# Performance work log

Hardware: AMD Instinct MI355X
Metric: run time of the kernel (lower is better)

Reference implementation:

```python
import jax, jax.numpy as jnp
import numpy as np

R = 65  # num_relations


def rgcn_conv(x, edge_index, edge_type, W, root, bias):
    """PyG RGCNConv with per-relation mean aggregation.
    Aggregate-then-transform (linearity lets us swap the order):
      mean_r[n] = mean over edges e with type r, dst(e)=n of x[src(e)]
      out = sum_r mean_r @ W_r + x @ root + bias
    """
    N = x.shape[0]
    src, dst = edge_index[0], edge_index[1]
    seg = edge_type * N + dst  # composite (relation, dst) segment id
    sums = jax.ops.segment_sum(x[src], seg, num_segments=R * N)
    sums = sums.reshape(R, N, -1)  # [R, N, F]
    cnt = jax.ops.segment_sum(jnp.ones(src.shape, x.dtype), seg, num_segments=R * N)
    cnt = cnt.reshape(R, N, 1)
    mean = sums / jnp.maximum(cnt, 1.0)
    return jnp.einsum('rni,rio->no', mean, W) + x @ root + bias


def setup_inputs() -> dict:
    key = jax.random.key(0)
    ks = jax.random.split(key, 20)
    N, E, F_in, H, M = 8000, 192000, 64, 256, 64
    B = 128
    inp = {
        'x': jax.random.normal(ks[0], (N, F_in), jnp.float32),
        'edge_index': jax.random.randint(ks[1], (2, E), 0, N),
        'edge_type': jax.random.randint(ks[2], (E,), 0, R),
        'batch': jnp.sort(jax.random.randint(ks[3], (N,), 0, B)),
    }
    def glorot(k, shape):
        fan = shape[-2] + shape[-1]
        return jax.random.normal(k, shape, jnp.float32) * jnp.sqrt(2.0 / fan)
    inp['W1'] = glorot(ks[4], (R, F_in, H)); inp['root1'] = glorot(ks[5], (F_in, H)); inp['b1'] = jnp.zeros((H,), jnp.float32)
    inp['W2'] = glorot(ks[6], (R, H, H));   inp['root2'] = glorot(ks[7], (H, H));   inp['b2'] = jnp.zeros((H,), jnp.float32)
    inp['W3'] = glorot(ks[8], (R, H, H));   inp['root3'] = glorot(ks[9], (H, H));   inp['b3'] = jnp.zeros((H,), jnp.float32)
    inp['ws_w'] = glorot(ks[10], (H, 1));    inp['ws_b'] = jnp.zeros((1,), jnp.float32)
    inp['m_w1'] = glorot(ks[11], (H, M)); inp['m_b1'] = jnp.zeros((M,), jnp.float32)
    inp['m_w2'] = glorot(ks[12], (M, M)); inp['m_b2'] = jnp.zeros((M,), jnp.float32)
    inp['m_w3'] = glorot(ks[13], (M, 1)); inp['m_b3'] = jnp.zeros((1,), jnp.float32)
    return inp


def reference(x, edge_index, edge_type, batch,
              W1, root1, b1, W2, root2, b2, W3, root3, b3,
              ws_w, ws_b, m_w1, m_b1, m_w2, m_b2, m_w3, m_b3):
    B = 128  # number of graphs in the batch
    h = jax.nn.relu(rgcn_conv(x, edge_index, edge_type, W1, root1, b1))
    h = jax.nn.relu(rgcn_conv(h, edge_index, edge_type, W2, root2, b2))
    h = jax.nn.relu(rgcn_conv(h, edge_index, edge_type, W3, root3, b3))
    # WeightedSum pooling: sigmoid gate per node, scatter-sum per graph
    w = jax.nn.sigmoid(h @ ws_w + ws_b)            # [N, 1]
    pooled = jax.ops.segment_sum(w * h, batch, num_segments=B)  # [B, H]
    # MLP head
    m = jax.nn.relu(pooled @ m_w1 + m_b1)
    m = jax.nn.relu(m @ m_w2 + m_b2)
    return m @ m_w3 + m_b3                          # [B, 1]
```

## Files before the change

### kernel.cpp

```cpp
#include <hip/hip_runtime.h>

#define NNODES 8000
#define NEDGES 192000
#define NREL   65
#define RP     66
#define HDIM   256
#define FDIM   64
#define NGRAPH 128
#define MDIM   64
#define TILE_M 64
#define MAXT   3456
#define EPTOT  (NEDGES + NNODES)

typedef _Float16 half8 __attribute__((ext_vector_type(8)));
typedef _Float16 half4 __attribute__((ext_vector_type(4)));
typedef float    f32x4 __attribute__((ext_vector_type(4)));


__global__ void count_kernel(const int* __restrict__ ei, const int* __restrict__ et,
                             int* __restrict__ cnt_rn, int* __restrict__ type_cnt,
                             int* __restrict__ ddeg) {
    __shared__ int lbin[NREL];
    int tid = threadIdx.x;
    if (tid < NREL) lbin[tid] = 0;
    __syncthreads();
    int e = blockIdx.x * 256 + tid;
    if (e < NEDGES) {
        int t = et[e];
        int d = ei[NEDGES + e];
        atomicAdd(&lbin[t], 1);
        atomicAdd(&cnt_rn[t * NNODES + d], 1);
        atomicAdd(&ddeg[d], 1);
    }
    __syncthreads();
    if (tid < NREL && lbin[tid] > 0) atomicAdd(&type_cnt[tid], lbin[tid]);
}

__global__ void scan_tiles_kernel(const int* __restrict__ type_cnt, int* __restrict__ type_off,
                                  int* __restrict__ tile_rel, int* __restrict__ tile_start,
                                  int* __restrict__ tile_nrows) {
    __shared__ int s_off[RP + 1];
    __shared__ int s_toff[RP + 1];
    if (threadIdx.x == 0) {
        int off = 0, toff = 0;
        for (int r = 0; r < RP; r++) {
            int c = (r < NREL) ? type_cnt[r] : NNODES;
            s_off[r] = off; s_toff[r] = toff;
            off += c; toff += (c + TILE_M - 1) / TILE_M;
        }
        s_off[RP] = off; s_toff[RP] = toff;
        type_off[RP] = off;
    }
    __syncthreads();
    int r = threadIdx.x;
    if (r < RP) {
        type_off[r] = s_off[r];
        int c = s_off[r + 1] - s_off[r];
        int nt = (c + TILE_M - 1) / TILE_M;
        for (int i = 0; i < nt; i++) {
            int idx = s_toff[r] + i;
            tile_rel[idx]   = r;
            tile_start[idx] = s_off[r] + i * TILE_M;
            tile_nrows[idx] = min(TILE_M, c - i * TILE_M);
        }
    }
}

__global__ void dst_scan_kernel(const int* __restrict__ ddeg, int* __restrict__ dst_off) {
    __shared__ int part[256];
    int t = threadIdx.x;
    int base = t * 32;
    int s = 0;
    for (int i = 0; i < 32; i++) {
        int n = base + i;
        if (n < NNODES) s += ddeg[n] + 1;
    }
    part[t] = s;
    __syncthreads();
    if (t == 0) {
        int run = 0;
        for (int i = 0; i < 256; i++) { int tmp = part[i]; part[i] = run; run += tmp; }
        dst_off[NNODES] = run;
    }
    __syncthreads();
    int run = part[t];
    for (int i = 0; i < 32; i++) {
        int n = base + i;
        if (n < NNODES) { dst_off[n] = run; run += ddeg[n] + 1; }
    }
}

__global__ void scatter_kernel(const int* __restrict__ ei, const int* __restrict__ et,
                               const int* __restrict__ cnt_rn, const int* __restrict__ type_off,
                               int* __restrict__ type_cur,
                               const int* __restrict__ dst_off, int* __restrict__ dst_cur,
                               int* __restrict__ esrc, int* __restrict__ eq,
                               float* __restrict__ escale) {
    __shared__ int lbin[NREL];
    __shared__ int gbase[NREL];
    int tid = threadIdx.x;
    if (tid < NREL) lbin[tid] = 0;
    __syncthreads();
    int i = blockIdx.x * 256 + tid;
    int t = 0, lrank = 0;
    bool is_edge = (i < NEDGES);
    if (is_edge) {
        t = et[i];
        lrank = atomicAdd(&lbin[t], 1);
    }
    __syncthreads();
    if (tid < NREL && lbin[tid] > 0) gbase[tid] = atomicAdd(&type_cur[tid], lbin[tid]);
    __syncthreads();
    if (is_edge) {
        int d = ei[NEDGES + i];
        int p = type_off[t] + gbase[t] + lrank;
        int q = dst_off[d] + atomicAdd(&dst_cur[d], 1);
        esrc[p] = ei[i];
        eq[p] = q;
        escale[p] = 1.0f / (float)cnt_rn[t * NNODES + d];
    } else if (i < EPTOT) {
        int n = i - NEDGES;
        int p = NEDGES + n;
        int q = dst_off[n] + atomicAdd(&dst_cur[n], 1);
        esrc[p] = n; eq[p] = q; escale[p] = 1.0f;
    }
}

__global__ void convW_kernel(const float* __restrict__ W, const float* __restrict__ root,
                             _Float16* __restrict__ Wt, int K) {
    int r = blockIdx.x, k0 = blockIdx.y * 32, n0 = blockIdx.z * 32;
    const float* src = (r < NREL) ? (W + (size_t)r * K * HDIM) : root;
    __shared__ float tile[32][33];
    int tj = threadIdx.x & 31, ti = threadIdx.x >> 5;
    #pragma unroll
    for (int s = 0; s < 4; s++) {
        int i = ti + s * 8;
        tile[i][tj] = src[(size_t)(k0 + i) * HDIM + n0 + tj];
    }
    __syncthreads();
    #pragma unroll
    for (int s = 0; s < 4; s++) {
        int i = ti + s * 8;
        Wt[((size_t)r * HDIM + (n0 + i)) * K + k0 + tj] = (_Float16)tile[tj][i];
    }
}

__global__ void conv_x_kernel(const float* __restrict__ x, _Float16* __restrict__ x16) {
    int i = blockIdx.x * 256 + threadIdx.x;
    if (i < NNODES * FDIM) x16[i] = (_Float16)x[i];
}

template <int K>
__global__ __launch_bounds__(256)
void edge_gemm_kernel(const _Float16* __restrict__ hin, const _Float16* __restrict__ Wt,
                      const int* __restrict__ esrc, const int* __restrict__ eq,
                      const float* __restrict__ escale,
                      const int* __restrict__ tile_rel, const int* __restrict__ tile_start,
                      const int* __restrict__ tile_nrows,
                      _Float16* __restrict__ Y) {
    int nr = tile_nrows[blockIdx.x];
    if (nr == 0) return;
    int r  = tile_rel[blockIdx.x];
    int ts = tile_start[blockIdx.x];

    constexpr int LK = K + 8;
    constexpr int SO = HDIM + 8;
    constexpr int LMAX = (LK > SO) ? LK : SO;
    __shared__ _Float16 sbuf[TILE_M * LMAX];
    __shared__ int   sq[TILE_M];
    __shared__ float sscale[TILE_M];

    int tid = threadIdx.x;
    constexpr int CPR = K / 8;
    for (int idx = tid; idx < TILE_M * CPR; idx += 256) {
        int row = idx / CPR, c = idx % CPR;
        uint4 v = make_uint4(0, 0, 0, 0);
        if (row < nr) {
            int src = esrc[ts + row];
            v = *(const uint4*)(hin + (size_t)src * K + c * 8);
        }
        *(uint4*)&sbuf[row * LK + c * 8] = v;
    }
    if (tid < TILE_M) {
        if (tid < nr) { sq[tid] = eq[ts + tid]; sscale[tid] = escale[ts + tid]; }
        else          { sq[tid] = 0;            sscale[tid] = 0.f; }
    }
    __syncthreads();

    int lane = tid & 63, w = tid >> 6;
    int lm = lane & 15, quad = lane >> 4;
    f32x4 acc[4][4] = {};
    const _Float16* Bbase = Wt + ((size_t)r * HDIM + w * 64 + lm) * K + quad * 8;
    const _Float16* Abase = sbuf + lm * LK + quad * 8;

    for (int kk = 0; kk < K; kk += 32) {
        half8 a[4], b[4];
        #pragma unroll
        for (int mt = 0; mt < 4; mt++)
            a[mt] = *(const half8*)(Abase + mt * 16 * LK + kk);
        #pragma unroll
        for (int nt = 0; nt < 4; nt++)
            b[nt] = *(const half8*)(Bbase + nt * 16 * K + kk);
        #pragma unroll
        for (int mt = 0; mt < 4; mt++)
            #pragma unroll
            for (int nt = 0; nt < 4; nt++)
                acc[mt][nt] = __builtin_amdgcn_mfma_f32_16x16x32_f16(a[mt], b[nt], acc[mt][nt], 0, 0, 0);
    }

    __syncthreads();

    #pragma unroll
    for (int mt = 0; mt < 4; mt++) {
        #pragma unroll
        for (int rr = 0; rr < 4; rr++) {
            int row = mt * 16 + quad * 4 + rr;
            float s = sscale[row];
            #pragma unroll
            for (int nt = 0; nt < 4; nt++) {
                int col = w * 64 + nt * 16 + lm;
                sbuf[row * SO + col] = (_Float16)(acc[mt][nt][rr] * s);
            }
        }
    }
    __syncthreads();

    for (int idx = tid; idx < TILE_M * 32; idx += 256) {
        int row = idx >> 5, seg = idx & 31;
        if (row < nr) {
            uint4 v = *(const uint4*)&sbuf[row * SO + seg * 8];
            *(uint4*)(Y + (size_t)sq[row] * HDIM + seg * 8) = v;
        }
    }
}

__global__ __launch_bounds__(256)
void reduce_kernel(const _Float16* __restrict__ Y, const int* __restrict__ dst_off,
                   const float* __restrict__ bias, _Float16* __restrict__ hout) {
    int n = blockIdx.x;
    int start = dst_off[n], end = dst_off[n + 1];
    int t = threadIdx.x;
    int c = t & 31;
    int r = t >> 5;
    float acc[8] = {0, 0, 0, 0, 0, 0, 0, 0};
    for (int j = start + r; j < end; j += 8) {
        half8 v = *(const half8*)(Y + (size_t)j * HDIM + c * 8);
        #pragma unroll
        for (int k = 0; k < 8; k++) acc[k] += (float)v[k];
    }
    __shared__ float red[8][32][8];
    #pragma unroll
    for (int k = 0; k < 8; k++) red[r][c][k] = acc[k];
    __syncthreads();
    if (t < 32) {
        float a[8];
        #pragma unroll
        for (int k = 0; k < 8; k++) a[k] = red[0][t][k];
        for (int rr = 1; rr < 8; rr++)
            #pragma unroll
            for (int k = 0; k < 8; k++) a[k] += red[rr][t][k];
        half8 o;
        #pragma unroll
        for (int k = 0; k < 8; k++) {
            float v = a[k] + bias[t * 8 + k];
            o[k] = (_Float16)(v > 0.f ? v : 0.f);
        }
        *(half8*)(hout + (size_t)n * HDIM + t * 8) = o;
    }
}


__global__ void gate_kernel(const _Float16* __restrict__ h, const float* __restrict__ ws_w,
                            const float* __restrict__ ws_b, float* __restrict__ gate) {
    int node = blockIdx.x * 4 + (threadIdx.x >> 6);
    int lane = threadIdx.x & 63;
    half4 v = *(const half4*)(h + (size_t)node * HDIM + lane * 4);
    float s = 0.f;
    #pragma unroll
    for (int k = 0; k < 4; k++) s += (float)v[k] * ws_w[lane * 4 + k];
    for (int o = 32; o > 0; o >>= 1) s += __shfl_down(s, o, 64);
    if (lane == 0) gate[node] = 1.f / (1.f + __expf(-(s + ws_b[0])));
}

__global__ void pool_kernel(const _Float16* __restrict__ h, const float* __restrict__ gate,
                            const int* __restrict__ batch, float* __restrict__ pooled) {
    int g = blockIdx.x, t = threadIdx.x;
    int a = 0, b = NNODES;
    while (a < b) { int m = (a + b) >> 1; if (batch[m] < g) a = m + 1; else b = m; }
    int lo = a;
    b = NNODES;
    while (a < b) { int m = (a + b) >> 1; if (batch[m] < g + 1) a = m + 1; else b = m; }
    int hi = a;
    float acc = 0.f;
    for (int n = lo; n < hi; n++)
        acc += gate[n] * (float)h[(size_t)n * HDIM + t];
    pooled[(size_t)g * HDIM + t] = acc;
}

__global__ void head_kernel(const float* __restrict__ pooled,
                            const float* __restrict__ w1, const float* __restrict__ b1,
                            const float* __restrict__ w2, const float* __restrict__ b2,
                            const float* __restrict__ w3, const float* __restrict__ b3,
                            float* __restrict__ out) {
    int b = blockIdx.x, tid = threadIdx.x;
    __shared__ float sp[HDIM];
    __shared__ float m1[MDIM];
    __shared__ float m2[MDIM];
    for (int i = tid; i < HDIM; i += 64) sp[i] = pooled[(size_t)b * HDIM + i];
    __syncthreads();
    float a = b1[tid];
    for (int i = 0; i < HDIM; i++) a += sp[i] * w1[i * MDIM + tid];
    m1[tid] = a > 0.f ? a : 0.f;
    __syncthreads();
    float c = b2[tid];
    for (int i = 0; i < MDIM; i++) c += m1[i] * w2[i * MDIM + tid];
    m2[tid] = c > 0.f ? c : 0.f;
    __syncthreads();
    float p = m2[tid] * w3[tid];
    for (int o = 32; o > 0; o >>= 1) p += __shfl_down(p, o, 64);
    if (tid == 0) out[b] = p + b3[0];
}


extern "C" void kernel_launch(void* const* d_in, const int* in_sizes, int n_in,
                              void* d_out, int out_size, void* d_ws, size_t ws_size,
                              hipStream_t stream) {
    const float* x     = (const float*)d_in[0];
    const int*   ei    = (const int*)d_in[1];
    const int*   et    = (const int*)d_in[2];
    const int*   batch = (const int*)d_in[3];
    const float* W1    = (const float*)d_in[4];
    const float* root1 = (const float*)d_in[5];
    const float* b1    = (const float*)d_in[6];
    const float* W2    = (const float*)d_in[7];
    const float* root2 = (const float*)d_in[8];
    const float* b2    = (const float*)d_in[9];
    const float* W3    = (const float*)d_in[10];
    const float* root3 = (const float*)d_in[11];
    const float* b3    = (const float*)d_in[12];
    const float* ws_w  = (const float*)d_in[13];
    const float* ws_b  = (const float*)d_in[14];
    const float* m_w1  = (const float*)d_in[15];
    const float* m_b1  = (const float*)d_in[16];
    const float* m_w2  = (const float*)d_in[17];
    const float* m_b2  = (const float*)d_in[18];
    const float* m_w3  = (const float*)d_in[19];
    const float* m_b3  = (const float*)d_in[20];
    float* out = (float*)d_out;

    char* ws = (char*)d_ws;
    size_t o = 0;
    auto take = [&](size_t bytes) { size_t r = o; o = (o + bytes + 255) & ~(size_t)255; return r; };

    size_t o_cnt_rn = take((size_t)NREL * NNODES * 4);
    size_t o_tcnt   = take(RP * 4);
    size_t o_tcur   = take(RP * 4);
    size_t o_toff   = take((RP + 1) * 4);
    size_t o_ddeg   = take((size_t)NNODES * 4);
    size_t o_dcur   = take((size_t)NNODES * 4);
    size_t o_doff   = take((size_t)(NNODES + 1) * 4);
    size_t o_esrc   = take((size_t)EPTOT * 4);
    size_t o_eq     = take((size_t)EPTOT * 4);
    size_t o_escale = take((size_t)EPTOT * 4);
    size_t o_trel   = take(MAXT * 4);
    size_t o_tstart = take(MAXT * 4);
    size_t o_tnrows = take(MAXT * 4);
    size_t o_wt1    = take((size_t)RP * HDIM * FDIM * 2);
    size_t o_wt2    = take((size_t)RP * HDIM * HDIM * 2);
    size_t o_wt3    = take((size_t)RP * HDIM * HDIM * 2);
    size_t o_x16    = take((size_t)NNODES * FDIM * 2);
    size_t o_h16    = take((size_t)NNODES * HDIM * 2);
    size_t o_gate   = take((size_t)NNODES * 4);
    size_t o_pool   = take((size_t)NGRAPH * HDIM * 4);
    size_t o_y16    = take((size_t)EPTOT * HDIM * 2);

    int*      cnt_rn   = (int*)(ws + o_cnt_rn);
    int*      type_cnt = (int*)(ws + o_tcnt);
    int*      type_cur = (int*)(ws + o_tcur);
    int*      type_off = (int*)(ws + o_toff);
    int*      ddeg     = (int*)(ws + o_ddeg);
    int*      dst_cur  = (int*)(ws + o_dcur);
    int*      dst_off  = (int*)(ws + o_doff);
    int*      esrc     = (int*)(ws + o_esrc);
    int*      eq       = (int*)(ws + o_eq);
    float*    escale   = (float*)(ws + o_escale);
    int*      trel     = (int*)(ws + o_trel);
    int*      tstart   = (int*)(ws + o_tstart);
    int*      tnrows   = (int*)(ws + o_tnrows);
    _Float16* Wt1      = (_Float16*)(ws + o_wt1);
    _Float16* Wt2      = (_Float16*)(ws + o_wt2);
    _Float16* Wt3      = (_Float16*)(ws + o_wt3);
    _Float16* x16      = (_Float16*)(ws + o_x16);
    _Float16* h16      = (_Float16*)(ws + o_h16);
    float*    gate     = (float*)(ws + o_gate);
    float*    pooled   = (float*)(ws + o_pool);
    _Float16* Y16      = (_Float16*)(ws + o_y16);

    hipMemsetAsync(ws + o_cnt_rn, 0, o_toff - o_cnt_rn, stream);
    hipMemsetAsync(ws + o_ddeg, 0, o_doff - o_ddeg, stream);
    hipMemsetAsync(ws + o_tnrows, 0, MAXT * 4, stream);

    count_kernel<<<(NEDGES + 255) / 256, 256, 0, stream>>>(ei, et, cnt_rn, type_cnt, ddeg);
    scan_tiles_kernel<<<1, 128, 0, stream>>>(type_cnt, type_off, trel, tstart, tnrows);
    dst_scan_kernel<<<1, 256, 0, stream>>>(ddeg, dst_off);
    scatter_kernel<<<(EPTOT + 255) / 256, 256, 0, stream>>>(ei, et, cnt_rn, type_off, type_cur,
                                                            dst_off, dst_cur, esrc, eq, escale);

    convW_kernel<<<dim3(RP, FDIM / 32, HDIM / 32), 256, 0, stream>>>(W1, root1, Wt1, FDIM);
    convW_kernel<<<dim3(RP, HDIM / 32, HDIM / 32), 256, 0, stream>>>(W2, root2, Wt2, HDIM);
    convW_kernel<<<dim3(RP, HDIM / 32, HDIM / 32), 256, 0, stream>>>(W3, root3, Wt3, HDIM);
    conv_x_kernel<<<(NNODES * FDIM + 255) / 256, 256, 0, stream>>>(x, x16);

    edge_gemm_kernel<FDIM><<<MAXT, 256, 0, stream>>>(x16, Wt1, esrc, eq, escale,
                                                     trel, tstart, tnrows, Y16);
    reduce_kernel<<<NNODES, 256, 0, stream>>>(Y16, dst_off, b1, h16);

    edge_gemm_kernel<HDIM><<<MAXT, 256, 0, stream>>>(h16, Wt2, esrc, eq, escale,
                                                     trel, tstart, tnrows, Y16);
    reduce_kernel<<<NNODES, 256, 0, stream>>>(Y16, dst_off, b2, h16);

    edge_gemm_kernel<HDIM><<<MAXT, 256, 0, stream>>>(h16, Wt3, esrc, eq, escale,
                                                     trel, tstart, tnrows, Y16);
    reduce_kernel<<<NNODES, 256, 0, stream>>>(Y16, dst_off, b3, h16);

    gate_kernel<<<NNODES / 4, 256, 0, stream>>>(h16, ws_w, ws_b, gate);
    pool_kernel<<<NGRAPH, 256, 0, stream>>>(h16, gate, batch, pooled);
    head_kernel<<<NGRAPH, 64, 0, stream>>>(pooled, m_w1, m_b1, m_w2, m_b2, m_w3, m_b3, out);

    (void)in_sizes; (void)n_in; (void)out_size; (void)ws_size;
}
```

Baseline: 490.9 us.

## Shrink edge GEMM LDS footprint, swizzle tile order, use nontemporal Y traffic

The edge GEMM kernel now stages the gathered A rows in K-chunks of at most 128 and writes the output tile back in two 32-row halves, which shrinks the shared-memory buffer and should allow more blocks per CU. The block-to-tile mapping is interleaved across eight strides, which spreads relations and tile sizes more evenly across the grid. Stores to Y and the loads in the reduce kernel now use nontemporal hints to avoid polluting cache with streamed intermediate data. The cost is extra barriers per chunk and half, and the interleaved mapping assumes the grid size equals MAXT.

Measured after the change: 503.9 us. 1.03x slower.

```diff
diff --git a/kernel.cpp b/kernel.cpp
--- a/kernel.cpp
+++ b/kernel.cpp
@@ -15,6 +15,7 @@
 typedef _Float16 half8 __attribute__((ext_vector_type(8)));
 typedef _Float16 half4 __attribute__((ext_vector_type(4)));
 typedef float    f32x4 __attribute__((ext_vector_type(4)));
+typedef unsigned int u32x4 __attribute__((ext_vector_type(4)));
 
 
 __global__ void count_kernel(const int* __restrict__ ei, const int* __restrict__ et,
@@ -158,34 +159,29 @@
                       const int* __restrict__ tile_rel, const int* __restrict__ tile_start,
                       const int* __restrict__ tile_nrows,
                       _Float16* __restrict__ Y) {
-    int nr = tile_nrows[blockIdx.x];
+    int bid  = blockIdx.x;
+    int tile = (bid & 7) * (MAXT / 8) + (bid >> 3);
+
+    int nr = tile_nrows[tile];
     if (nr == 0) return;
-    int r  = tile_rel[blockIdx.x];
-    int ts = tile_start[blockIdx.x];
-
-    constexpr int LK = K + 8;
-    constexpr int SO = HDIM + 8;
-    constexpr int LMAX = (LK > SO) ? LK : SO;
-    __shared__ _Float16 sbuf[TILE_M * LMAX];
+    int r  = tile_rel[tile];
+    int ts = tile_start[tile];
+
+    constexpr int KH  = (K > 128) ? 128 : K;
+    constexpr int LK  = KH + 8;
+    constexpr int SO  = HDIM + 8;
+    constexpr int AEL = TILE_M * LK;
+    constexpr int OEL = 32 * SO;
+    constexpr int EL  = (AEL > OEL) ? AEL : OEL;
+    __shared__ _Float16 sbuf[EL];
     __shared__ int   sq[TILE_M];
     __shared__ float sscale[TILE_M];
 
     int tid = threadIdx.x;
-    constexpr int CPR = K / 8;
-    for (int idx = tid; idx < TILE_M * CPR; idx += 256) {
-        int row = idx / CPR, c = idx % CPR;
-        uint4 v = make_uint4(0, 0, 0, 0);
-        if (row < nr) {
-            int src = esrc[ts + row];
-            v = *(const uint4*)(hin + (size_t)src * K + c * 8);
-        }
-        *(uint4*)&sbuf[row * LK + c * 8] = v;
-    }
     if (tid < TILE_M) {
         if (tid < nr) { sq[tid] = eq[ts + tid]; sscale[tid] = escale[ts + tid]; }
         else          { sq[tid] = 0;            sscale[tid] = 0.f; }
     }
-    __syncthreads();
 
     int lane = tid & 63, w = tid >> 6;
     int lm = lane & 15, quad = lane >> 4;
@@ -193,44 +189,63 @@
     const _Float16* Bbase = Wt + ((size_t)r * HDIM + w * 64 + lm) * K + quad * 8;
     const _Float16* Abase = sbuf + lm * LK + quad * 8;
 
-    for (int kk = 0; kk < K; kk += 32) {
-        half8 a[4], b[4];
-        #pragma unroll
-        for (int mt = 0; mt < 4; mt++)
-            a[mt] = *(const half8*)(Abase + mt * 16 * LK + kk);
-        #pragma unroll
-        for (int nt = 0; nt < 4; nt++)
-            b[nt] = *(const half8*)(Bbase + nt * 16 * K + kk);
-        #pragma unroll
-        for (int mt = 0; mt < 4; mt++)
+    constexpr int CPR = KH / 8;
+    for (int kh = 0; kh < K; kh += KH) {
+        for (int idx = tid; idx < TILE_M * CPR; idx += 256) {
+            int row = idx / CPR, c = idx % CPR;
+            u32x4 v = {0, 0, 0, 0};
+            if (row < nr) {
+                int src = esrc[ts + row];
+                v = *(const u32x4*)(hin + (size_t)src * K + kh + c * 8);
+            }
+            *(u32x4*)&sbuf[row * LK + c * 8] = v;
+        }
+        __syncthreads();
+
+        for (int kk = 0; kk < KH; kk += 32) {
+            half8 a[4], b[4];
+            #pragma unroll
+            for (int mt = 0; mt < 4; mt++)
+                a[mt] = *(const half8*)(Abase + mt * 16 * LK + kk);
             #pragma unroll
             for (int nt = 0; nt < 4; nt++)
-                acc[mt][nt] = __builtin_amdgcn_mfma_f32_16x16x32_f16(a[mt], b[nt], acc[mt][nt], 0, 0, 0);
-    }
-
-    __syncthreads();
+                b[nt] = *(const half8*)(Bbase + nt * 16 * K + kh + kk);
+            #pragma unroll
+            for (int mt = 0; mt < 4; mt++)
+                #pragma unroll
+                for (int nt = 0; nt < 4; nt++)
+                    acc[mt][nt] = __builtin_amdgcn_mfma_f32_16x16x32_f16(a[mt], b[nt], acc[mt][nt], 0, 0, 0);
+        }
+        __syncthreads();
+    }
 
     #pragma unroll
-    for (int mt = 0; mt < 4; mt++) {
+    for (int h = 0; h < 2; h++) {
         #pragma unroll
-        for (int rr = 0; rr < 4; rr++) {
-            int row = mt * 16 + quad * 4 + rr;
-            float s = sscale[row];
+        for (int mh = 0; mh < 2; mh++) {
+            int mt = h * 2 + mh;
             #pragma unroll
-            for (int nt = 0; nt < 4; nt++) {
-                int col = w * 64 + nt * 16 + lm;
-                sbuf[row * SO + col] = (_Float16)(acc[mt][nt][rr] * s);
+            for (int rr = 0; rr < 4; rr++) {
+                int row  = mt * 16 + quad * 4 + rr;
+                int lrow = row - h * 32;
+                float s = sscale[row];
+                #pragma unroll
+                for (int nt = 0; nt < 4; nt++) {
+                    int col = w * 64 + nt * 16 + lm;
+                    sbuf[lrow * SO + col] = (_Float16)(acc[mt][nt][rr] * s);
+                }
             }
         }
-    }
-    __syncthreads();
-
-    for (int idx = tid; idx < TILE_M * 32; idx += 256) {
-        int row = idx >> 5, seg = idx & 31;
-        if (row < nr) {
-            uint4 v = *(const uint4*)&sbuf[row * SO + seg * 8];
-            *(uint4*)(Y + (size_t)sq[row] * HDIM + seg * 8) = v;
-        }
+        __syncthreads();
+        for (int idx = tid; idx < 32 * 32; idx += 256) {
+            int lrow = idx >> 5, seg = idx & 31;
+            int row = h * 32 + lrow;
+            if (row < nr) {
+                u32x4 v = *(const u32x4*)&sbuf[lrow * SO + seg * 8];
+                __builtin_nontemporal_store(v, (u32x4*)(Y + (size_t)sq[row] * HDIM + seg * 8));
+            }
+        }
+        if (h == 0) __syncthreads();
     }
 }
 
@@ -244,7 +259,8 @@
     int r = t >> 5;
     float acc[8] = {0, 0, 0, 0, 0, 0, 0, 0};
     for (int j = start + r; j < end; j += 8) {
-        half8 v = *(const half8*)(Y + (size_t)j * HDIM + c * 8);
+        u32x4 u = __builtin_nontemporal_load((const u32x4*)(Y + (size_t)j * HDIM + c * 8));
+        half8 v = *(half8*)&u;
         #pragma unroll
         for (int k = 0; k < 8; k++) acc[k] += (float)v[k];
     }
```

## Load gathered A rows directly from global and use per-wave epilogue scratch

Applied to the files above, without the earlier changes.

The edge GEMM stops staging gathered source rows in shared memory and has each lane load its A fragments straight from global memory via per-row source indices. The epilogue writes into a per-wave scratch buffer, so no block-wide barriers are needed, and Y is written and read with nontemporal stores and loads. Tile order is also swizzled across block ids, and launch bounds request three blocks per CU. This removes the LDS staging pass and the syncs, but every wave now re-reads the gathered rows from global or cache.

After: 615.5 us. +25.4%, slower.

```diff
diff --git a/kernel.cpp b/kernel.cpp
--- a/kernel.cpp
+++ b/kernel.cpp
@@ -15,6 +15,7 @@
 typedef _Float16 half8 __attribute__((ext_vector_type(8)));
 typedef _Float16 half4 __attribute__((ext_vector_type(4)));
 typedef float    f32x4 __attribute__((ext_vector_type(4)));
+typedef unsigned int u32x4 __attribute__((ext_vector_type(4)));
 
 
 __global__ void count_kernel(const int* __restrict__ ei, const int* __restrict__ et,
@@ -151,56 +152,44 @@
 }
 
 template <int K>
-__global__ __launch_bounds__(256)
+__global__ __launch_bounds__(256, 3)
 void edge_gemm_kernel(const _Float16* __restrict__ hin, const _Float16* __restrict__ Wt,
                       const int* __restrict__ esrc, const int* __restrict__ eq,
                       const float* __restrict__ escale,
                       const int* __restrict__ tile_rel, const int* __restrict__ tile_start,
                       const int* __restrict__ tile_nrows,
                       _Float16* __restrict__ Y) {
-    int nr = tile_nrows[blockIdx.x];
+    int bid  = blockIdx.x;
+    int tile = (bid & 7) * (MAXT / 8) + (bid >> 3);
+
+    int nr = tile_nrows[tile];
     if (nr == 0) return;
-    int r  = tile_rel[blockIdx.x];
-    int ts = tile_start[blockIdx.x];
-
-    constexpr int LK = K + 8;
-    constexpr int SO = HDIM + 8;
-    constexpr int LMAX = (LK > SO) ? LK : SO;
-    __shared__ _Float16 sbuf[TILE_M * LMAX];
-    __shared__ int   sq[TILE_M];
-    __shared__ float sscale[TILE_M];
+    int r  = tile_rel[tile];
+    int ts = tile_start[tile];
 
     int tid = threadIdx.x;
-    constexpr int CPR = K / 8;
-    for (int idx = tid; idx < TILE_M * CPR; idx += 256) {
-        int row = idx / CPR, c = idx % CPR;
-        uint4 v = make_uint4(0, 0, 0, 0);
-        if (row < nr) {
-            int src = esrc[ts + row];
-            v = *(const uint4*)(hin + (size_t)src * K + c * 8);
-        }
-        *(uint4*)&sbuf[row * LK + c * 8] = v;
-    }
-    if (tid < TILE_M) {
-        if (tid < nr) { sq[tid] = eq[ts + tid]; sscale[tid] = escale[ts + tid]; }
-        else          { sq[tid] = 0;            sscale[tid] = 0.f; }
-    }
-    __syncthreads();
-
     int lane = tid & 63, w = tid >> 6;
     int lm = lane & 15, quad = lane >> 4;
+
+    int srcr[4];
+    #pragma unroll
+    for (int mt = 0; mt < 4; mt++) {
+        int row = mt * 16 + lm;
+        srcr[mt] = (row < nr) ? esrc[ts + row] : 0;
+    }
+
+    const _Float16* Bb = Wt + ((size_t)r * HDIM + w * 64 + lm) * K + quad * 8;
+
     f32x4 acc[4][4] = {};
-    const _Float16* Bbase = Wt + ((size_t)r * HDIM + w * 64 + lm) * K + quad * 8;
-    const _Float16* Abase = sbuf + lm * LK + quad * 8;
-
+    #pragma unroll
     for (int kk = 0; kk < K; kk += 32) {
         half8 a[4], b[4];
         #pragma unroll
         for (int mt = 0; mt < 4; mt++)
-            a[mt] = *(const half8*)(Abase + mt * 16 * LK + kk);
+            a[mt] = *(const half8*)(hin + (size_t)srcr[mt] * K + kk + quad * 8);
         #pragma unroll
         for (int nt = 0; nt < 4; nt++)
-            b[nt] = *(const half8*)(Bbase + nt * 16 * K + kk);
+            b[nt] = *(const half8*)(Bb + nt * 16 * K + kk);
         #pragma unroll
         for (int mt = 0; mt < 4; mt++)
             #pragma unroll
@@ -208,28 +197,26 @@
                 acc[mt][nt] = __builtin_amdgcn_mfma_f32_16x16x32_f16(a[mt], b[nt], acc[mt][nt], 0, 0, 0);
     }
 
-    __syncthreads();
-
+    __shared__ _Float16 scr[4][64][72];
     #pragma unroll
     for (int mt = 0; mt < 4; mt++) {
         #pragma unroll
         for (int rr = 0; rr < 4; rr++) {
             int row = mt * 16 + quad * 4 + rr;
-            float s = sscale[row];
+            float s = (row < nr) ? escale[ts + row] : 0.f;
             #pragma unroll
-            for (int nt = 0; nt < 4; nt++) {
-                int col = w * 64 + nt * 16 + lm;
-                sbuf[row * SO + col] = (_Float16)(acc[mt][nt][rr] * s);
-            }
+            for (int nt = 0; nt < 4; nt++)
+                scr[w][row][nt * 16 + lm] = (_Float16)(acc[mt][nt][rr] * s);
         }
     }
-    __syncthreads();
-
-    for (int idx = tid; idx < TILE_M * 32; idx += 256) {
-        int row = idx >> 5, seg = idx & 31;
+    #pragma unroll
+    for (int j = 0; j < 8; j++) {
+        int idx = j * 64 + lane;
+        int row = idx >> 3, ck = idx & 7;
         if (row < nr) {
-            uint4 v = *(const uint4*)&sbuf[row * SO + seg * 8];
-            *(uint4*)(Y + (size_t)sq[row] * HDIM + seg * 8) = v;
+            int q = eq[ts + row];
+            u32x4 v = *(const u32x4*)&scr[w][row][ck * 8];
+            __builtin_nontemporal_store(v, (u32x4*)(Y + (size_t)q * HDIM + w * 64 + ck * 8));
         }
     }
 }
@@ -244,7 +231,8 @@
     int r = t >> 5;
     float acc[8] = {0, 0, 0, 0, 0, 0, 0, 0};
     for (int j = start + r; j < end; j += 8) {
-        half8 v = *(const half8*)(Y + (size_t)j * HDIM + c * 8);
+        u32x4 u = __builtin_nontemporal_load((const u32x4*)(Y + (size_t)j * HDIM + c * 8));
+        half8 v = *(half8*)&u;
         #pragma unroll
         for (int k = 0; k < 8; k++) acc[k] += (float)v[k];
     }
```
